# Kernel tuning notes

Hardware: AMD Instinct MI355X
Metric: run time of the kernel (lower is better)

The kernel has to match this reference:

```python
import jax, jax.numpy as jnp
import numpy as np

B = 2            # batch_size (number of windows)
W_SIZE = 2       # window_size
WIDTH = 256      # cart_pixel_width
TEMP = 0.01      # softmax_temp
EPS = 1e-12      # F.normalize eps


def _l2norm(x, axis):
    n = jnp.sqrt(jnp.sum(x * x, axis=axis, keepdims=True))
    return x / jnp.maximum(n, EPS)


def _bilinear(img, u, v):
    """align_corners=True bilinear sample. img: [C,H,W]; u,v: [N] pixel coords."""
    H, W = img.shape[-2], img.shape[-1]
    u0 = jnp.clip(jnp.floor(u), 0, W - 1)
    v0 = jnp.clip(jnp.floor(v), 0, H - 1)
    u1 = jnp.clip(u0 + 1, 0, W - 1)
    v1 = jnp.clip(v0 + 1, 0, H - 1)
    au = u - u0
    av = v - v0
    u0i, u1i = u0.astype(jnp.int32), u1.astype(jnp.int32)
    v0i, v1i = v0.astype(jnp.int32), v1.astype(jnp.int32)
    g = lambda vi, ui: img[:, vi, ui]  # [C,N]
    return (g(v0i, u0i) * (1 - au) * (1 - av) + g(v0i, u1i) * au * (1 - av)
            + g(v1i, u0i) * (1 - au) * av + g(v1i, u1i) * au * av)


def setup_inputs() -> dict:
    key = jax.random.key(0)
    k1, k2, k3, k4 = jax.random.split(key, 4)
    BW, C, N, S = B * W_SIZE, 248, 1024, 1
    return {
        "keypoint_scores": jax.random.normal(k1, (BW, S, N), dtype=jnp.float32),
        "keypoint_desc": jax.random.normal(k2, (BW, C, N), dtype=jnp.float32),
        "desc_dense": jax.random.normal(k3, (BW, C, WIDTH, WIDTH), dtype=jnp.float32),
        "times_img": jax.random.uniform(k4, (BW, 1, WIDTH, WIDTH), dtype=jnp.float32),
    }


def reference(keypoint_scores, keypoint_desc, desc_dense, times_img):
    BW, C, N = keypoint_desc.shape
    w = W_SIZE
    # frame index bookkeeping (same as the torch per-batch loop, vectorized)
    src_ids = jnp.arange(B) * w                                   # [B]
    tgt_ids = (jnp.arange(B)[:, None] * w
               + jnp.arange(1, w)[None, :]).reshape(-1)           # [B*(w-1)]

    # dense pixel coordinates [W^2, 2] in (u, v) order
    v, u = jnp.meshgrid(jnp.arange(WIDTH), jnp.arange(WIDTH), indexing='ij')
    coords = jnp.stack([u.reshape(-1), v.reshape(-1)], axis=1).astype(desc_dense.dtype)

    # normalized source dense descriptors [B, C, W^2]
    src = _l2norm(desc_dense[src_ids].reshape(B, C, -1), axis=1)
    # normalized target keypoint descriptors [B, w-1, C, N]
    tgt = _l2norm(keypoint_desc[tgt_ids].reshape(B, w - 1, C, N), axis=2)

    # dense correlation: [B, w-1, N, W^2]
    match_vals = jnp.einsum('bkcn,bcm->bknm', tgt, src)
    soft = jax.nn.softmax(match_vals / TEMP, axis=-1)
    # coordinate-weighted sum -> pseudo coords [B*(w-1), N, 2]
    pseudo_coords = jnp.einsum('bknm,md->bknd', soft, coords).reshape(B * (w - 1), N, 2)

    # bilinear-sample src times at pseudo coords (normalize->grid_sample round trip
    # with align_corners maps back to the same pixel coords; H == W here)
    src_times = jnp.repeat(times_img[src_ids], w - 1, axis=0)      # [B*(w-1),1,H,W]
    pseudo_times = jax.vmap(_bilinear)(src_times,
                                       pseudo_coords[..., 0],
                                       pseudo_coords[..., 1])      # [B*(w-1),1,N]

    return (pseudo_coords, keypoint_scores[tgt_ids], tgt_ids, pseudo_times)
```

## Files before the change

kernel.cpp:

```cpp
#include <hip/hip_runtime.h>
#include <math.h>

typedef int i32x4 __attribute__((ext_vector_type(4)));
typedef int i32x16 __attribute__((ext_vector_type(16)));

#define CC 248
#define MM 65536
#define NN 1024

__device__ __forceinline__ float fexp2(float x) { return __builtin_amdgcn_exp2f(x); }


__global__ __launch_bounds__(256)
void convA_kernel(const float* __restrict__ kdesc, char* __restrict__ Bg) {
    __shared__ char bt[2][16][32][16];
    __shared__ float scr[8][32];
    const int bid = blockIdx.x;
    const int b   = bid >> 5;
    const int nt  = bid & 31;
    const int n0  = nt * 32;
    const int tid = threadIdx.x;
    const int col = tid & 31;
    const int q   = tid >> 5;

    const float* kp = kdesc + (size_t)(2 * b + 1) * CC * NN + n0 + col;
    float ss = 0.f;
    for (int i = 0; i < 31; ++i) {
        int c = q * 31 + i;
        float v = kp[(size_t)c * NN];
        ss += v * v;
    }
    scr[q][col] = ss;
    __syncthreads();
    float tot = 0.f;
#pragma unroll
    for (int k = 0; k < 8; ++k) tot += scr[k][col];
    float inv = 32768.0f / fmaxf(sqrtf(tot), 1e-12f);
    if (tid < 64) {
        int pl = tid >> 5, c2 = tid & 31;
        *(long*)&bt[pl][15][c2][8] = 0L;
    }
    __syncthreads();
    for (int i = 0; i < 31; ++i) {
        int c = q * 31 + i;
        float qq = fminf(fmaxf(rintf(kp[(size_t)c * NN] * inv), -32768.f), 32639.f);
        int af = (int)qq;
        int a1 = (af + 128) >> 8;
        int a0 = af - (a1 << 8);
        bt[0][c >> 4][col][c & 15] = (char)a1;
        bt[1][c >> 4][col][c & 15] = (char)a0;
    }
    __syncthreads();
    char* outb = Bg + (size_t)(b * 32 + nt) * 16384;
    const char* src = &bt[0][0][0][0];
#pragma unroll
    for (int it = 0; it < 4; ++it) {
        int id = tid + it * 256;
        *(i32x4*)&outb[(size_t)id * 16] = *(const i32x4*)&src[(size_t)id * 16];
    }
}

__global__ __launch_bounds__(256, 2)
void fused_kernel(const float* __restrict__ dense, const char* __restrict__ Bg,
                  float* __restrict__ partials) {
    extern __shared__ char lds[];
    float* scr = (float*)(lds + 65536);

    const int bid = blockIdx.x;
    const int fb  = bid >> 9;
    const int p0  = (bid & 511) * 128;
    const int tid = threadIdx.x;

    {
        const int row = tid & 127;
        const int q   = tid >> 7;
        const float* dptr = dense + (size_t)(2 * fb) * CC * MM + (size_t)(q * 124) * MM + p0 + row;
        float v[124];
        float ss = 0.f;
#pragma unroll
        for (int i = 0; i < 124; ++i) {
            v[i] = dptr[(size_t)i * MM];
            ss += v[i] * v[i];
        }
        scr[q * 128 + row] = ss;
        *(long*)&lds[(tid >> 7) * 32768 + 15 * 2048 + (tid & 127) * 16 + 8] = 0L;
        __syncthreads();
        float inv = 32768.0f / fmaxf(sqrtf(scr[row] + scr[128 + row]), 1e-12f);
#pragma unroll
        for (int j = 0; j < 31; ++j) {
            unsigned w1 = 0, w0 = 0;
#pragma unroll
            for (int t = 0; t < 4; ++t) {
                float qv = fminf(fmaxf(rintf(v[j * 4 + t] * inv), -32768.f), 32639.f);
                int af = (int)qv;
                int a1 = (af + 128) >> 8;
                int a0 = af - (a1 << 8);
                w1 |= (unsigned)(a1 & 255) << (8 * t);
                w0 |= (unsigned)(a0 & 255) << (8 * t);
            }
            int c0 = q * 124 + j * 4;
            int kg = c0 >> 4, dw = (c0 >> 2) & 3;
            *(unsigned*)&lds[kg * 2048 + row * 16 + dw * 4] = w1;
            *(unsigned*)&lds[32768 + kg * 2048 + row * 16 + dw * 4] = w0;
        }
    }
    __syncthreads();

    const int lane = tid & 63;
    const int w    = tid >> 6;
    const int lrow = lane & 31;
    const int lhi  = lane >> 5;

    const char* bbase = Bg + (size_t)(fb * 32) * 16384;

    const float S2 = 100.0f * 1.4426950408889634f / 1073741824.0f;
    const float cH = 65536.0f * S2;
    const float cX = 256.0f * S2;
    const float BASE = 145.0f;

    for (int nc = 0; nc < 4; ++nc) {
        i32x4 bc[8][2][2];
#pragma unroll
        for (int kk = 0; kk < 8; ++kk)
#pragma unroll
            for (int pl = 0; pl < 2; ++pl)
#pragma unroll
                for (int bp = 0; bp < 2; ++bp)
                    bc[kk][pl][bp] = *(const i32x4*)(bbase
                        + (size_t)(w * 8 + nc * 2 + bp) * 16384 + pl * 8192
                        + (kk * 2 + lhi) * 512 + lrow * 16);

        float rz[2] = {0.f, 0.f}, rsu[2] = {0.f, 0.f}, rsv[2] = {0.f, 0.f};

#pragma unroll
        for (int mt = 0; mt < 4; ++mt) {
            i32x16 accH[2], accX[2];
#pragma unroll
            for (int bp = 0; bp < 2; ++bp) { accH[bp] = (i32x16)(0); accX[bp] = (i32x16)(0); }

#pragma unroll
            for (int kk = 0; kk < 8; ++kk) {
                i32x4 a1 = *(const i32x4*)&lds[(kk * 2 + lhi) * 2048 + (mt * 32 + lrow) * 16];
                i32x4 a0 = *(const i32x4*)&lds[32768 + (kk * 2 + lhi) * 2048 + (mt * 32 + lrow) * 16];
                __builtin_amdgcn_s_setprio(1);
#pragma unroll
                for (int bp = 0; bp < 2; ++bp) {
                    accH[bp] = __builtin_amdgcn_mfma_i32_32x32x32_i8(a1, bc[kk][0][bp], accH[bp], 0, 0, 0);
                    accX[bp] = __builtin_amdgcn_mfma_i32_32x32x32_i8(a1, bc[kk][1][bp], accX[bp], 0, 0, 0);
                    accX[bp] = __builtin_amdgcn_mfma_i32_32x32x32_i8(a0, bc[kk][0][bp], accX[bp], 0, 0, 0);
                }
                __builtin_amdgcn_s_setprio(0);
            }

            const int mbase = p0 + mt * 32;
            const float ub = (float)((mbase & 255) + 4 * lhi);
            const float vcoord = (float)(mbase >> 8);
#pragma unroll
            for (int bp = 0; bp < 2; ++bp) {
                float tz = 0.f, tsur = 0.f;
#pragma unroll
                for (int r = 0; r < 16; ++r) {
                    float e = fexp2(fmaf((float)accH[bp][r], cH,
                                    fmaf((float)accX[bp][r], cX, -BASE)));
                    tz += e;
                    tsur = fmaf(e, (float)((r & 3) + 8 * (r >> 2)), tsur);
                }
                rz[bp] += tz;
                rsu[bp] += fmaf(ub, tz, tsur);
                rsv[bp] = fmaf(vcoord, tz, rsv[bp]);
            }
        }

#pragma unroll
        for (int bp = 0; bp < 2; ++bp) {
            rz[bp]  += __shfl_xor(rz[bp],  32, 64);
            rsu[bp] += __shfl_xor(rsu[bp], 32, 64);
            rsv[bp] += __shfl_xor(rsv[bp], 32, 64);
        }
        if (lane < 32) {
#pragma unroll
            for (int bp = 0; bp < 2; ++bp) {
                int n = w * 256 + nc * 64 + bp * 32 + lrow;
                size_t idxp = ((size_t)(fb * NN + n)) * 512 + (bid & 511);
                ((float4*)partials)[idxp] = make_float4(rz[bp], rsu[bp], rsv[bp], 0.f);
            }
        }
    }
}

__global__ __launch_bounds__(256)
void combine_kernel(const float* __restrict__ partials,
                    const float* __restrict__ kscores,
                    const float* __restrict__ times,
                    float* __restrict__ out) {
    const int wg   = blockIdx.x * 4 + (threadIdx.x >> 6);
    const int lane = threadIdx.x & 63;
    const int b = wg >> 10, n = wg & 1023;
    const float4* pp = (const float4*)partials + (size_t)wg * 512;

    float z = 0.f, su = 0.f, sv = 0.f;
#pragma unroll
    for (int k = 0; k < 8; ++k) {
        float4 p = pp[k * 64 + lane];
        z += p.x; su += p.y; sv += p.z;
    }
#pragma unroll
    for (int mask = 32; mask >= 1; mask >>= 1) {
        z  += __shfl_xor(z,  mask, 64);
        su += __shfl_xor(su, mask, 64);
        sv += __shfl_xor(sv, mask, 64);
    }

    if (lane == 0) {
        float u = su / z, v = sv / z;
        out[(size_t)wg * 2 + 0] = u;
        out[(size_t)wg * 2 + 1] = v;
        out[4096 + wg] = kscores[(size_t)(2 * b + 1) * NN + n];
        if (wg == 0) { out[6144] = 1.0f; out[6145] = 3.0f; }

        const float* timg = times + (size_t)(2 * b) * MM;
        float u0 = fminf(fmaxf(floorf(u), 0.f), 255.f);
        float v0 = fminf(fmaxf(floorf(v), 0.f), 255.f);
        float u1 = fminf(u0 + 1.f, 255.f);
        float v1 = fminf(v0 + 1.f, 255.f);
        float au = u - u0, av = v - v0;
        int u0i = (int)u0, u1i = (int)u1, v0i = (int)v0, v1i = (int)v1;
        float t00 = timg[v0i * 256 + u0i], t01 = timg[v0i * 256 + u1i];
        float t10 = timg[v1i * 256 + u0i], t11 = timg[v1i * 256 + u1i];
        float t = t00 * (1.f - au) * (1.f - av) + t01 * au * (1.f - av)
                + t10 * (1.f - au) * av + t11 * au * av;
        out[6146 + wg] = t;
    }
}

extern "C" void kernel_launch(void* const* d_in, const int* in_sizes, int n_in,
                              void* d_out, int out_size, void* d_ws, size_t ws_size,
                              hipStream_t stream) {
    const float* kscores = (const float*)d_in[0];
    const float* kdesc   = (const float*)d_in[1];
    const float* dense   = (const float*)d_in[2];
    const float* times   = (const float*)d_in[3];
    float* out = (float*)d_out;

    char* Bg = (char*)d_ws;
    float* partials = (float*)(Bg + (size_t)2 * 32 * 16384);

    hipFuncSetAttribute((const void*)fused_kernel,
                        hipFuncAttributeMaxDynamicSharedMemorySize, 66560);

    hipLaunchKernelGGL(convA_kernel,   dim3(64),   dim3(256), 0, stream, kdesc, Bg);
    hipLaunchKernelGGL(fused_kernel,   dim3(1024), dim3(256), 66560, stream, dense, Bg, partials);
    hipLaunchKernelGGL(combine_kernel, dim3(512),  dim3(256), 0, stream, partials, kscores, times, out);
}
```

Measured before the change: 120.4 us.

## Process two pixel tiles per block, overlapping next tile's norm loads with MFMA

Measured after the change: 138.5 us. 15.0% more time.

```diff
diff --git a/kernel.cpp b/kernel.cpp
--- a/kernel.cpp
+++ b/kernel.cpp
@@ -64,126 +64,148 @@
 void fused_kernel(const float* __restrict__ dense, const char* __restrict__ Bg,
                   float* __restrict__ partials) {
     extern __shared__ char lds[];
-    float* scr = (float*)(lds + 65536);
-
-    const int bid = blockIdx.x;
-    const int fb  = bid >> 9;
-    const int p0  = (bid & 511) * 128;
-    const int tid = threadIdx.x;
-
-    {
-        const int row = tid & 127;
-        const int q   = tid >> 7;
-        const float* dptr = dense + (size_t)(2 * fb) * CC * MM + (size_t)(q * 124) * MM + p0 + row;
-        float v[124];
-        float ss = 0.f;
-#pragma unroll
-        for (int i = 0; i < 124; ++i) {
-            v[i] = dptr[(size_t)i * MM];
-            ss += v[i] * v[i];
-        }
-        scr[q * 128 + row] = ss;
-        *(long*)&lds[(tid >> 7) * 32768 + 15 * 2048 + (tid & 127) * 16 + 8] = 0L;
-        __syncthreads();
-        float inv = 32768.0f / fmaxf(sqrtf(scr[row] + scr[128 + row]), 1e-12f);
+
+    const int bid   = blockIdx.x;
+    const int fb    = bid >> 8;
+    const int local = bid & 255;
+
+    const int tid  = threadIdx.x;
+    const int row  = tid >> 1;
+    const int half = tid & 1;
+
+    const int lane = tid & 63;
+    const int w    = tid >> 6;
+    const int lrow = lane & 31;
+    const int lhi  = lane >> 5;
+
+    const float* dbase = dense + (size_t)(2 * fb) * CC * MM + (size_t)(half * 124) * MM + row;
+    const char*  bbase = Bg + (size_t)(fb * 32) * 16384;
+
+    const float S2 = 100.0f * 1.4426950408889634f / 1073741824.0f;
+    const float cH = 65536.0f * S2;
+    const float cX = 256.0f * S2;
+    const float BASE = 145.0f;
+
+    auto PASSA_CHUNK = [&](int p, int chunk, float& ss) {
+        const float* dp = dbase + (local * 2 + p) * 128 + (size_t)(chunk * 31) * MM;
+#pragma unroll
+        for (int i = 0; i < 31; ++i) {
+            float x = dp[(size_t)i * MM];
+            ss = fmaf(x, x, ss);
+        }
+    };
+
+    auto PASSB = [&](int p, float inv) {
+        const float* dp = dbase + (local * 2 + p) * 128;
+        *(long*)&lds[half * 32768 + 15 * 2048 + row * 16 + 8] = 0L;
 #pragma unroll
         for (int j = 0; j < 31; ++j) {
             unsigned w1 = 0, w0 = 0;
 #pragma unroll
             for (int t = 0; t < 4; ++t) {
-                float qv = fminf(fmaxf(rintf(v[j * 4 + t] * inv), -32768.f), 32639.f);
+                float x = dp[(size_t)(j * 4 + t) * MM];
+                float qv = fminf(fmaxf(rintf(x * inv), -32768.f), 32639.f);
                 int af = (int)qv;
                 int a1 = (af + 128) >> 8;
                 int a0 = af - (a1 << 8);
                 w1 |= (unsigned)(a1 & 255) << (8 * t);
                 w0 |= (unsigned)(a0 & 255) << (8 * t);
             }
-            int c0 = q * 124 + j * 4;
+            int c0 = half * 124 + j * 4;
             int kg = c0 >> 4, dw = (c0 >> 2) & 3;
             *(unsigned*)&lds[kg * 2048 + row * 16 + dw * 4] = w1;
             *(unsigned*)&lds[32768 + kg * 2048 + row * 16 + dw * 4] = w0;
         }
-    }
-    __syncthreads();
-
-    const int lane = tid & 63;
-    const int w    = tid >> 6;
-    const int lrow = lane & 31;
-    const int lhi  = lane >> 5;
-
-    const char* bbase = Bg + (size_t)(fb * 32) * 16384;
-
-    const float S2 = 100.0f * 1.4426950408889634f / 1073741824.0f;
-    const float cH = 65536.0f * S2;
-    const float cX = 256.0f * S2;
-    const float BASE = 145.0f;
-
-    for (int nc = 0; nc < 4; ++nc) {
-        i32x4 bc[8][2][2];
-#pragma unroll
-        for (int kk = 0; kk < 8; ++kk)
-#pragma unroll
-            for (int pl = 0; pl < 2; ++pl)
-#pragma unroll
-                for (int bp = 0; bp < 2; ++bp)
-                    bc[kk][pl][bp] = *(const i32x4*)(bbase
-                        + (size_t)(w * 8 + nc * 2 + bp) * 16384 + pl * 8192
-                        + (kk * 2 + lhi) * 512 + lrow * 16);
-
-        float rz[2] = {0.f, 0.f}, rsu[2] = {0.f, 0.f}, rsv[2] = {0.f, 0.f};
-
-#pragma unroll
-        for (int mt = 0; mt < 4; ++mt) {
-            i32x16 accH[2], accX[2];
-#pragma unroll
-            for (int bp = 0; bp < 2; ++bp) { accH[bp] = (i32x16)(0); accX[bp] = (i32x16)(0); }
-
-#pragma unroll
-            for (int kk = 0; kk < 8; ++kk) {
-                i32x4 a1 = *(const i32x4*)&lds[(kk * 2 + lhi) * 2048 + (mt * 32 + lrow) * 16];
-                i32x4 a0 = *(const i32x4*)&lds[32768 + (kk * 2 + lhi) * 2048 + (mt * 32 + lrow) * 16];
-                __builtin_amdgcn_s_setprio(1);
+    };
+
+    float ssn = 0.f;
+#pragma unroll
+    for (int c = 0; c < 4; ++c) PASSA_CHUNK(0, c, ssn);
+    float ss1 = 0.f;
+
+#pragma unroll
+    for (int p = 0; p < 2; ++p) {
+        float tot = ssn + __shfl_xor(ssn, 1, 64);
+        float inv = 32768.0f / fmaxf(sqrtf(tot), 1e-12f);
+        PASSB(p, inv);
+        __syncthreads();
+
+        const int pp0 = (local * 2 + p) * 128;
+
+        for (int nc = 0; nc < 4; ++nc) {
+            if (p == 0) PASSA_CHUNK(1, nc, ss1);
+
+            i32x4 bc[8][2][2];
+#pragma unroll
+            for (int kk = 0; kk < 8; ++kk)
+#pragma unroll
+                for (int pl = 0; pl < 2; ++pl)
+#pragma unroll
+                    for (int bp = 0; bp < 2; ++bp)
+                        bc[kk][pl][bp] = *(const i32x4*)(bbase
+                            + (size_t)(w * 8 + nc * 2 + bp) * 16384 + pl * 8192
+                            + (kk * 2 + lhi) * 512 + lrow * 16);
+
+            float rz[2] = {0.f, 0.f}, rsu[2] = {0.f, 0.f}, rsv[2] = {0.f, 0.f};
+
+#pragma unroll
+            for (int mt = 0; mt < 4; ++mt) {
+                i32x16 accH[2], accX[2];
+#pragma unroll
+                for (int bp = 0; bp < 2; ++bp) { accH[bp] = (i32x16)(0); accX[bp] = (i32x16)(0); }
+
+#pragma unroll
+                for (int kk = 0; kk < 8; ++kk) {
+                    i32x4 a1 = *(const i32x4*)&lds[(kk * 2 + lhi) * 2048 + (mt * 32 + lrow) * 16];
+                    i32x4 a0 = *(const i32x4*)&lds[32768 + (kk * 2 + lhi) * 2048 + (mt * 32 + lrow) * 16];
+                    __builtin_amdgcn_s_setprio(1);
+#pragma unroll
+                    for (int bp = 0; bp < 2; ++bp) {
+                        accH[bp] = __builtin_amdgcn_mfma_i32_32x32x32_i8(a1, bc[kk][0][bp], accH[bp], 0, 0, 0);
+                        accX[bp] = __builtin_amdgcn_mfma_i32_32x32x32_i8(a1, bc[kk][1][bp], accX[bp], 0, 0, 0);
+                        accX[bp] = __builtin_amdgcn_mfma_i32_32x32x32_i8(a0, bc[kk][0][bp], accX[bp], 0, 0, 0);
+                    }
+                    __builtin_amdgcn_s_setprio(0);
+                }
+
+                const int mbase = pp0 + mt * 32;
+                const float ub = (float)((mbase & 255) + 4 * lhi);
+                const float vcoord = (float)(mbase >> 8);
 #pragma unroll
                 for (int bp = 0; bp < 2; ++bp) {
-                    accH[bp] = __builtin_amdgcn_mfma_i32_32x32x32_i8(a1, bc[kk][0][bp], accH[bp], 0, 0, 0);
-                    accX[bp] = __builtin_amdgcn_mfma_i32_32x32x32_i8(a1, bc[kk][1][bp], accX[bp], 0, 0, 0);
-                    accX[bp] = __builtin_amdgcn_mfma_i32_32x32x32_i8(a0, bc[kk][0][bp], accX[bp], 0, 0, 0);
+                    float tz = 0.f, tsur = 0.f;
+#pragma unroll
+                    for (int r = 0; r < 16; ++r) {
+                        float e = fexp2(fmaf((float)accH[bp][r], cH,
+                                        fmaf((float)accX[bp][r], cX, -BASE)));
+                        tz += e;
+                        tsur = fmaf(e, (float)((r & 3) + 8 * (r >> 2)), tsur);
+                    }
+                    rz[bp] += tz;
+                    rsu[bp] += fmaf(ub, tz, tsur);
+                    rsv[bp] = fmaf(vcoord, tz, rsv[bp]);
                 }
-                __builtin_amdgcn_s_setprio(0);
-            }
-
-            const int mbase = p0 + mt * 32;
-            const float ub = (float)((mbase & 255) + 4 * lhi);
-            const float vcoord = (float)(mbase >> 8);
+            }
+
 #pragma unroll
             for (int bp = 0; bp < 2; ++bp) {
-                float tz = 0.f, tsur = 0.f;
-#pragma unroll
-                for (int r = 0; r < 16; ++r) {
-                    float e = fexp2(fmaf((float)accH[bp][r], cH,
-                                    fmaf((float)accX[bp][r], cX, -BASE)));
-                    tz += e;
-                    tsur = fmaf(e, (float)((r & 3) + 8 * (r >> 2)), tsur);
+                rz[bp]  += __shfl_xor(rz[bp],  32, 64);
+                rsu[bp] += __shfl_xor(rsu[bp], 32, 64);
+                rsv[bp] += __shfl_xor(rsv[bp], 32, 64);
+            }
+            if (lane < 32) {
+#pragma unroll
+                for (int bp = 0; bp < 2; ++bp) {
+                    int n = w * 256 + nc * 64 + bp * 32 + lrow;
+                    size_t idxp = ((size_t)(fb * NN + n)) * 512 + (local * 2 + p);
+                    ((float4*)partials)[idxp] = make_float4(rz[bp], rsu[bp], rsv[bp], 0.f);
                 }
-                rz[bp] += tz;
-                rsu[bp] += fmaf(ub, tz, tsur);
-                rsv[bp] = fmaf(vcoord, tz, rsv[bp]);
-            }
-        }
-
-#pragma unroll
-        for (int bp = 0; bp < 2; ++bp) {
-            rz[bp]  += __shfl_xor(rz[bp],  32, 64);
-            rsu[bp] += __shfl_xor(rsu[bp], 32, 64);
-            rsv[bp] += __shfl_xor(rsv[bp], 32, 64);
-        }
-        if (lane < 32) {
-#pragma unroll
-            for (int bp = 0; bp < 2; ++bp) {
-                int n = w * 256 + nc * 64 + bp * 32 + lrow;
-                size_t idxp = ((size_t)(fb * NN + n)) * 512 + (bid & 511);
-                ((float4*)partials)[idxp] = make_float4(rz[bp], rsu[bp], rsv[bp], 0.f);
-            }
+            }
+        }
+
+        if (p == 0) {
+            __syncthreads();
+            ssn = ss1;
         }
     }
 }
@@ -246,9 +268,9 @@
     float* partials = (float*)(Bg + (size_t)2 * 32 * 16384);
 
     hipFuncSetAttribute((const void*)fused_kernel,
-                        hipFuncAttributeMaxDynamicSharedMemorySize, 66560);
+                        hipFuncAttributeMaxDynamicSharedMemorySize, 65536);
 
     hipLaunchKernelGGL(convA_kernel,   dim3(64),   dim3(256), 0, stream, kdesc, Bg);
-    hipLaunchKernelGGL(fused_kernel,   dim3(1024), dim3(256), 66560, stream, dense, Bg, partials);
+    hipLaunchKernelGGL(fused_kernel,   dim3(512),  dim3(256), 65536, stream, dense, Bg, partials);
     hipLaunchKernelGGL(combine_kernel, dim3(512),  dim3(256), 0, stream, partials, kscores, times, out);
 }
```
